# Kernel optimization log

Hardware: AMD Instinct MI355X
Metric: run time of the kernel (lower is better)

Reference implementation:

```python
import jax, jax.numpy as jnp
import numpy as np

B, D, FV, EMB, HID, E = 256, 1000, 300, 128, 128, 32000
NUM_LAYERS = 3


def _gcn_layer(h, src, tgt, W, b):
    # PyG GCNConv (add_self_loops=True, normalize=True) over N = h.shape[0] nodes.
    # NOTE: edges only reference nodes [0, D) (faithful to original forward),
    # but self-loops exist for all N nodes.
    N = h.shape[0]
    h = h @ W.T  # [N, out]
    deg = jnp.ones((N,), h.dtype).at[tgt].add(1.0)  # self-loop + in-degree
    dinv = deg ** -0.5
    coef = dinv[src] * dinv[tgt]  # [E]
    agg = jnp.zeros_like(h).at[tgt].add(h[src] * coef[:, None])
    agg = agg + h * (dinv * dinv)[:, None]  # self-loop messages
    return agg + b


def setup_inputs() -> dict:
    key = jax.random.key(0)
    ks = jax.random.split(key, 10)
    inp = {
        "X_num": jax.random.normal(ks[0], (B, 800), jnp.float32),
        "X_cat": jax.random.normal(ks[1], (B, 200), jnp.float32),
        "V": jax.random.normal(ks[2], (D, FV), jnp.float32),
        "edge_index": jax.random.randint(ks[3], (2, E), 0, D, jnp.int32),
        "W_embed": jax.random.normal(ks[4], (EMB, FV), jnp.float32) / np.sqrt(FV),
        "b_embed": jnp.zeros((EMB,), jnp.float32),
        "W0": jax.random.normal(ks[5], (HID, EMB), jnp.float32) / np.sqrt(EMB),
        "b0": jnp.zeros((HID,), jnp.float32),
        "W1": jax.random.normal(ks[6], (HID, HID), jnp.float32) / np.sqrt(HID),
        "b1": jnp.zeros((HID,), jnp.float32),
        "W2": jax.random.normal(ks[7], (HID, HID), jnp.float32) / np.sqrt(HID),
        "b2": jnp.zeros((HID,), jnp.float32),
    }
    return inp


def reference(X_num, X_cat, V, edge_index, W_embed, b_embed, W0, b0, W1, b1, W2, b2):
    x = jnp.concatenate([X_num, X_cat], axis=1)  # [B, D]
    emb = V @ W_embed.T + b_embed  # [D, EMB]
    h = x[:, :, None] * emb[None, :, :]  # [B, D, EMB]
    h = h.reshape(B * D, EMB)
    src, tgt = edge_index[0], edge_index[1]
    for W, b in ((W0, b0), (W1, b1), (W2, b2)):
        h = jax.nn.relu(_gcn_layer(h, src, tgt, W, b))
    h = h.reshape(B, D, HID)
    return h.mean(axis=1)  # conv_pool_method == 'mean'
```

## Files before the change

### kernel.cpp

```cpp
#include <hip/hip_runtime.h>
#include <hip/hip_bf16.h>

#define B_N 256
#define D_N 1000
#define H_N 128
#define E_N 32000
#define CAP 128

typedef unsigned int uint32;
typedef unsigned short u16;
typedef __attribute__((ext_vector_type(8))) short bf16x8;
typedef __attribute__((ext_vector_type(4))) float f32x4;

__device__ __forceinline__ u16 f2bf(float f) {
    union { float f; uint32 u; } v; v.f = f;
    return (u16)((v.u + 0x7fffu + ((v.u >> 16) & 1u)) >> 16);
}
__device__ __forceinline__ uint32 pk2(float lo, float hi) {
    __hip_bfloat162 h = __float22bfloat162_rn(make_float2(lo, hi));
    union { __hip_bfloat162 h; uint32 u; } v; v.h = h; return v.u;
}
__device__ __forceinline__ float asf(uint32 u) {
    union { uint32 u; float f; } v; v.u = u; return v.f;
}
__device__ __forceinline__ float rl(float x) { return x > 0.f ? x : 0.f; }

__device__ __forceinline__ void ld8g(const float* __restrict__ p, int kbase, float v[8]) {
    if (kbase + 8 <= 300) {
        float4 a = *(const float4*)p, b = *(const float4*)(p + 4);
        v[0] = a.x; v[1] = a.y; v[2] = a.z; v[3] = a.w;
        v[4] = b.x; v[5] = b.y; v[6] = b.z; v[7] = b.w;
    } else {
#pragma unroll
        for (int j = 0; j < 8; ++j) v[j] = (kbase + j < 300) ? p[j] : 0.f;
    }
}

__global__ void k_prep(const float* __restrict__ V, const float* __restrict__ W_embed,
                       const float* __restrict__ b_embed, const float* __restrict__ W0,
                       const float* __restrict__ Xn, const float* __restrict__ Xc,
                       const float* __restrict__ W1, const float* __restrict__ W2,
                       int* __restrict__ deg,
                       u16* __restrict__ w1h, u16* __restrict__ w2h,
                       u16* __restrict__ E1h, float* __restrict__ t0,
                       float* __restrict__ out) {
    __shared__ __align__(16) u16 sW0[128 * 128];
    __shared__ __align__(16) u16 sWc[128 * 64];
    __shared__ __align__(16) u16 sVc[16 * 64];
    __shared__ __align__(16) u16 sT[16 * 128];

    int bid = blockIdx.x, tid = threadIdx.x;
    if (bid >= 63) {
        if (bid < 127) {
            int i = (bid - 63) * 256 + tid;
            w1h[i] = f2bf(W1[i]); w2h[i] = f2bf(W2[i]);
        } else if (bid < 255) {
            int i = (bid - 127) * 256 + tid;
            out[i] = 0.f;
        } else {
            for (int j = tid; j < D_N; j += 256) deg[j] = 0;
        }
        return;
    }

    const int wave = tid >> 6, lane = tid & 63;
    const int quad = lane >> 4, l15 = lane & 15;
    const int nh = wave;
    const int dbase = bid * 16;

#pragma unroll
    for (int ii = 0; ii < 8; ++ii) {
        int idx = tid + ii * 256;
        int row = idx >> 4, g = idx & 15;
        float4 a = *(const float4*)(W0 + row * 128 + g * 8);
        float4 b = *(const float4*)(W0 + row * 128 + g * 8 + 4);
        uint4 pk = { pk2(a.x, a.y), pk2(a.z, a.w), pk2(b.x, b.y), pk2(b.z, b.w) };
        *(uint4*)&sW0[row * 128 + ((g ^ (row & 7)) << 3)] = pk;
    }

    f32x4 accA[2];
#pragma unroll
    for (int n = 0; n < 2; ++n) { accA[n][0] = 0.f; accA[n][1] = 0.f; accA[n][2] = 0.f; accA[n][3] = 0.f; }

    for (int ck = 0; ck < 5; ++ck) {
        int k0 = ck * 64;
        if (tid < 128) {
            int row = tid >> 3, seg = tid & 7;
            int d = dbase + row; int dc = d < D_N ? d : D_N - 1;
            int kk = k0 + seg * 8;
            float v[8]; ld8g(V + dc * 300 + kk, kk, v);
            uint4 pk = { pk2(v[0], v[1]), pk2(v[2], v[3]), pk2(v[4], v[5]), pk2(v[6], v[7]) };
            *(uint4*)&sVc[row * 64 + ((seg ^ (row & 7)) << 3)] = pk;
        }
#pragma unroll
        for (int gg = 0; gg < 4; ++gg) {
            int idx = tid + gg * 256;
            int row = idx >> 3, g = idx & 7;
            int kk = k0 + g * 8;
            float v[8]; ld8g(W_embed + row * 300 + kk, kk, v);
            uint4 pk = { pk2(v[0], v[1]), pk2(v[2], v[3]), pk2(v[4], v[5]), pk2(v[6], v[7]) };
            *(uint4*)&sWc[row * 64 + ((g ^ (row & 7)) << 3)] = pk;
        }
        __syncthreads();
#pragma unroll
        for (int ksb = 0; ksb < 2; ++ksb) {
            int g = ksb * 4 + quad;
            int ar = l15;
            bf16x8 av = *(const bf16x8*)&sVc[ar * 64 + ((g ^ (ar & 7)) << 3)];
#pragma unroll
            for (int n = 0; n < 2; ++n) {
                int br = nh * 32 + n * 16 + l15;
                bf16x8 bv = *(const bf16x8*)&sWc[br * 64 + ((g ^ (br & 7)) << 3)];
                accA[n] = __builtin_amdgcn_mfma_f32_16x16x32_bf16(av, bv, accA[n], 0, 0, 0);
            }
        }
        __syncthreads();
    }

    {
        const int odd = l15 & 1;
#pragma unroll
        for (int n = 0; n < 2; ++n) {
            float bb = b_embed[nh * 32 + n * 16 + l15];
            float v0 = accA[n][0] + bb, v1 = accA[n][1] + bb;
            float v2 = accA[n][2] + bb, v3 = accA[n][3] + bb;
            float t0_ = __shfl_xor(v0, 1), t1_ = __shfl_xor(v1, 1);
            float t2_ = __shfl_xor(v2, 1), t3_ = __shfl_xor(v3, 1);
            float lo0 = odd ? t2_ : v0, hi0 = odd ? v2 : t0_;
            float lo1 = odd ? t3_ : v1, hi1 = odd ? v3 : t1_;
            int r0 = quad * 4 + (odd ? 2 : 0);
            int r1 = r0 + 1;
            int ce = nh * 32 + n * 16 + (l15 & ~1);
            *(uint32*)&sT[r0 * 128 + (((ce >> 3) ^ (r0 & 7)) << 3) + (ce & 7)] = pk2(lo0, hi0);
            *(uint32*)&sT[r1 * 128 + (((ce >> 3) ^ (r1 & 7)) << 3) + (ce & 7)] = pk2(lo1, hi1);
        }
    }
    __syncthreads();

    f32x4 accB[2];
#pragma unroll
    for (int n = 0; n < 2; ++n) { accB[n][0] = 0.f; accB[n][1] = 0.f; accB[n][2] = 0.f; accB[n][3] = 0.f; }
#pragma unroll
    for (int ks = 0; ks < 4; ++ks) {
        int g = ks * 4 + quad;
        int ar = l15;
        bf16x8 av = *(const bf16x8*)&sT[ar * 128 + ((g ^ (ar & 7)) << 3)];
#pragma unroll
        for (int n = 0; n < 2; ++n) {
            int br = nh * 32 + n * 16 + l15;
            bf16x8 bv = *(const bf16x8*)&sW0[br * 128 + ((g ^ (br & 7)) << 3)];
            accB[n] = __builtin_amdgcn_mfma_f32_16x16x32_bf16(av, bv, accB[n], 0, 0, 0);
        }
    }

#pragma unroll
    for (int i = 0; i < 4; ++i) {
        int r = quad * 4 + i;
        int d = dbase + r;
        if (d < D_N) {
            float x0 = (d < 800) ? Xn[d] : Xc[d - 800];
#pragma unroll
            for (int n = 0; n < 2; ++n) {
                int col = nh * 32 + n * 16 + l15;
                float e1 = accB[n][i];
                E1h[d * H_N + col] = f2bf(e1);
                t0[d * H_N + col] = x0 * e1;
            }
        }
    }
}

__global__ void k_layer(const float* __restrict__ t_in, const float* __restrict__ bias,
                        const float* __restrict__ Wn, const int* __restrict__ deg,
                        const int* __restrict__ es,
                        float* __restrict__ t_out, float* out, int pool) {
    __shared__ float sh[128];
    int d = blockIdx.x, e = threadIdx.x;
    float di = rsqrtf(1.f + (float)deg[d]);
    float acc = t_in[d * H_N + e] * di * di;
    int n = deg[d]; if (n > CAP) n = CAP;
    const int* row = es + d * CAP;
    int i = 0;
    for (; i + 4 <= n; i += 4) {
        int a0 = row[i], a1 = row[i + 1], a2 = row[i + 2], a3 = row[i + 3];
        float c0 = rsqrtf(1.f + (float)deg[a0]);
        float c1 = rsqrtf(1.f + (float)deg[a1]);
        float c2 = rsqrtf(1.f + (float)deg[a2]);
        float c3 = rsqrtf(1.f + (float)deg[a3]);
        acc += di * (c0 * t_in[a0 * H_N + e] + c1 * t_in[a1 * H_N + e] +
                     c2 * t_in[a2 * H_N + e] + c3 * t_in[a3 * H_N + e]);
    }
    for (; i < n; ++i) {
        int s = row[i];
        acc += di * rsqrtf(1.f + (float)deg[s]) * t_in[s * H_N + e];
    }
    float h = rl(acc + bias[e]);
    if (pool) { atomicAdd(&out[e], h * (1.0f / 1000.0f)); return; }
    sh[e] = h;
    __syncthreads();
    const float4* hr = (const float4*)sh;
    const float4* wr = (const float4*)(Wn + e * 128);
    float s = 0.f;
#pragma unroll 8
    for (int k = 0; k < 32; ++k) {
        float4 a = hr[k], w = wr[k];
        s += a.x * w.x + a.y * w.y + a.z * w.z + a.w * w.w;
    }
    t_out[d * H_N + e] = s;
}

__global__ __launch_bounds__(256, 4)
void k_big(const float* __restrict__ Xn, const float* __restrict__ Xc,
           const u16* __restrict__ E1h, const u16* __restrict__ w1h,
           const u16* __restrict__ w2h, const float* __restrict__ b0,
           const float* __restrict__ b1, const float* __restrict__ b2,
           const int* __restrict__ eidx, int* __restrict__ deg,
           int* __restrict__ es, float* __restrict__ out) {
    __shared__ __align__(16) u16 sH[4 * 32 * 128];

    if (blockIdx.x < 125) {
        int e = blockIdx.x * 256 + threadIdx.x;
        int s = eidx[e], t = eidx[E_N + e];
        int pos = atomicAdd(&deg[t], 1);
        if (pos < CAP) es[t * CAP + pos] = s;
        return;
    }
    const int cb = blockIdx.x - 125;
    const int tid = threadIdx.x;
    const int wave = tid >> 6, lane = tid & 63;
    const int quad = lane >> 4, l15 = lane & 15;
    const int bi = 1 + (cb >> 3);
    const int mbase = ((cb & 7) << 7) + wave * 32;
    u16* hw = sH + wave * (32 * 128);

    const int rA = mbase + l15;  const int rAc = rA < D_N ? rA : D_N - 1;
    const int rB = rA + 16;      const int rBc = rB < D_N ? rB : D_N - 1;
    const float xvA = (rAc < 800) ? Xn[bi * 800 + rAc] : Xc[bi * 200 + rAc - 800];
    const float xvB = (rBc < 800) ? Xn[bi * 800 + rBc] : Xc[bi * 200 + rBc - 800];

    f32x4 acc[2][8];
#pragma unroll
    for (int rt = 0; rt < 2; ++rt)
#pragma unroll
        for (int n = 0; n < 8; ++n) {
            acc[rt][n][0] = 0.f; acc[rt][n][1] = 0.f;
            acc[rt][n][2] = 0.f; acc[rt][n][3] = 0.f;
        }

#pragma unroll
    for (int ks = 0; ks < 4; ++ks) {
        const int k8 = ks * 4 + quad;
        uint4 eA = *(const uint4*)(E1h + rAc * H_N + k8 * 8);
        uint4 eB = *(const uint4*)(E1h + rBc * H_N + k8 * 8);
        float4 bl = *(const float4*)(b0 + k8 * 8);
        float4 bh = *(const float4*)(b0 + k8 * 8 + 4);
        uint4 pA, pB;
        {
            float a0 = rl(fmaf(xvA, asf(eA.x << 16), bl.x));
            float a1 = rl(fmaf(xvA, asf(eA.x & 0xffff0000u), bl.y));
            float a2 = rl(fmaf(xvA, asf(eA.y << 16), bl.z));
            float a3 = rl(fmaf(xvA, asf(eA.y & 0xffff0000u), bl.w));
            float a4 = rl(fmaf(xvA, asf(eA.z << 16), bh.x));
            float a5 = rl(fmaf(xvA, asf(eA.z & 0xffff0000u), bh.y));
            float a6 = rl(fmaf(xvA, asf(eA.w << 16), bh.z));
            float a7 = rl(fmaf(xvA, asf(eA.w & 0xffff0000u), bh.w));
            pA = { pk2(a0, a1), pk2(a2, a3), pk2(a4, a5), pk2(a6, a7) };
            float c0 = rl(fmaf(xvB, asf(eB.x << 16), bl.x));
            float c1 = rl(fmaf(xvB, asf(eB.x & 0xffff0000u), bl.y));
            float c2 = rl(fmaf(xvB, asf(eB.y << 16), bl.z));
            float c3 = rl(fmaf(xvB, asf(eB.y & 0xffff0000u), bl.w));
            float c4 = rl(fmaf(xvB, asf(eB.z << 16), bh.x));
            float c5 = rl(fmaf(xvB, asf(eB.z & 0xffff0000u), bh.y));
            float c6 = rl(fmaf(xvB, asf(eB.w << 16), bh.z));
            float c7 = rl(fmaf(xvB, asf(eB.w & 0xffff0000u), bh.w));
            pB = { pk2(c0, c1), pk2(c2, c3), pk2(c4, c5), pk2(c6, c7) };
        }
        bf16x8 aA = *(const bf16x8*)&pA;
        bf16x8 aB = *(const bf16x8*)&pB;
#pragma unroll
        for (int n = 0; n < 8; ++n) {
            bf16x8 bw = *(const bf16x8*)(w1h + (n * 16 + l15) * H_N + k8 * 8);
            acc[0][n] = __builtin_amdgcn_mfma_f32_16x16x32_bf16(aA, bw, acc[0][n], 0, 0, 0);
            acc[1][n] = __builtin_amdgcn_mfma_f32_16x16x32_bf16(aB, bw, acc[1][n], 0, 0, 0);
        }
    }

    {
        const int odd = l15 & 1;
#pragma unroll
        for (int rt = 0; rt < 2; ++rt)
#pragma unroll
            for (int n = 0; n < 8; ++n) {
                float bg = b1[n * 16 + l15];
                float v0 = rl(acc[rt][n][0] + bg);
                float v1 = rl(acc[rt][n][1] + bg);
                float v2 = rl(acc[rt][n][2] + bg);
                float v3 = rl(acc[rt][n][3] + bg);
                float t0_ = __shfl_xor(v0, 1), t1_ = __shfl_xor(v1, 1);
                float t2_ = __shfl_xor(v2, 1), t3_ = __shfl_xor(v3, 1);
                float lo0 = odd ? t2_ : v0, hi0 = odd ? v2 : t0_;
                float lo1 = odd ? t3_ : v1, hi1 = odd ? v3 : t1_;
                int r0 = rt * 16 + quad * 4 + (odd ? 2 : 0);
                int r1 = r0 + 1;
                int ce = n * 16 + (l15 & ~1);
                *(uint32*)&hw[r0 * 128 + (((ce >> 3) ^ (r0 & 7)) << 3) + (ce & 7)] = pk2(lo0, hi0);
                *(uint32*)&hw[r1 * 128 + (((ce >> 3) ^ (r1 & 7)) << 3) + (ce & 7)] = pk2(lo1, hi1);
            }
    }

#pragma unroll
    for (int rt = 0; rt < 2; ++rt)
#pragma unroll
        for (int n = 0; n < 8; ++n) {
            acc[rt][n][0] = 0.f; acc[rt][n][1] = 0.f;
            acc[rt][n][2] = 0.f; acc[rt][n][3] = 0.f;
        }
#pragma unroll
    for (int ks = 0; ks < 4; ++ks) {
        int k8 = ks * 4 + quad;
        int m0 = l15, m1 = 16 + l15;
        bf16x8 a0 = *(const bf16x8*)&hw[m0 * 128 + ((k8 ^ (m0 & 7)) << 3)];
        bf16x8 a1 = *(const bf16x8*)&hw[m1 * 128 + ((k8 ^ (m1 & 7)) << 3)];
#pragma unroll
        for (int n = 0; n < 8; ++n) {
            bf16x8 bw = *(const bf16x8*)(w2h + (n * 16 + l15) * H_N + k8 * 8);
            acc[0][n] = __builtin_amdgcn_mfma_f32_16x16x32_bf16(a0, bw, acc[0][n], 0, 0, 0);
            acc[1][n] = __builtin_amdgcn_mfma_f32_16x16x32_bf16(a1, bw, acc[1][n], 0, 0, 0);
        }
    }

    int rem = D_N - mbase;
#pragma unroll
    for (int n = 0; n < 8; ++n) {
        float bg = b2[n * 16 + l15];
        float cs = 0.f;
#pragma unroll
        for (int rt = 0; rt < 2; ++rt)
#pragma unroll
            for (int i = 0; i < 4; ++i) {
                int r32 = rt * 16 + quad * 4 + i;
                float v = rl(acc[rt][n][i] + bg);
                if (r32 < rem) cs += v;
            }
        cs += __shfl_xor(cs, 16);
        cs += __shfl_xor(cs, 32);
        if (lane < 16) atomicAdd(&out[bi * H_N + n * 16 + l15], cs * (1.0f / 1000.0f));
    }
}

extern "C" void kernel_launch(void* const* d_in, const int* in_sizes, int n_in,
                              void* d_out, int out_size, void* d_ws, size_t ws_size,
                              hipStream_t stream) {
    const float* Xn = (const float*)d_in[0];
    const float* Xc = (const float*)d_in[1];
    const float* V = (const float*)d_in[2];
    const int* eidx = (const int*)d_in[3];
    const float* W_embed = (const float*)d_in[4];
    const float* b_embed = (const float*)d_in[5];
    const float* W0 = (const float*)d_in[6];
    const float* b0 = (const float*)d_in[7];
    const float* W1 = (const float*)d_in[8];
    const float* b1 = (const float*)d_in[9];
    const float* W2 = (const float*)d_in[10];
    const float* b2 = (const float*)d_in[11];
    float* out = (float*)d_out;

    char* p = (char*)d_ws;
    auto alloc = [&](size_t bytes) -> char* {
        char* r = p;
        p += (bytes + 255) & ~(size_t)255;
        return r;
    };
    u16*   E1h = (u16*)  alloc(D_N * H_N * 2);
    float* t0  = (float*)alloc(D_N * H_N * 4);
    float* t1  = (float*)alloc(D_N * H_N * 4);
    float* t2  = (float*)alloc(D_N * H_N * 4);
    u16*   w1h = (u16*)  alloc(H_N * H_N * 2);
    u16*   w2h = (u16*)  alloc(H_N * H_N * 2);
    int*   deg = (int*)  alloc(D_N * 4);
    int*   es  = (int*)  alloc(D_N * CAP * 4);

    k_prep<<<dim3(256), dim3(256), 0, stream>>>(V, W_embed, b_embed, W0, Xn, Xc,
                                                W1, W2, deg, w1h, w2h, E1h, t0, out);
    k_big<<<dim3(2165), dim3(256), 0, stream>>>(Xn, Xc, E1h, w1h, w2h, b0, b1, b2,
                                                eidx, deg, es, out);
    k_layer<<<dim3(1000), dim3(128), 0, stream>>>(t0, b0, W1, deg, es, t1, out, 0);
    k_layer<<<dim3(1000), dim3(128), 0, stream>>>(t1, b1, W2, deg, es, t2, out, 0);
    k_layer<<<dim3(1000), dim3(128), 0, stream>>>(t2, b2, (const float*)nullptr, deg, es,
                                                  (float*)nullptr, out, 1);
}
```

Measured before the change: 226.4 us.

## Fuse all stages into one persistent kernel with software grid barriers

Replaces the prep, big-MLP, and three GCN layer launches with a single persistent kernel of 512 blocks that synchronize through atomic grid barriers. W1 and W2 bf16 weights are staged in shared memory rather than read from global memory, and layer phases now process two nodes per 256-thread block. This removes inter-launch gaps and tail effects at the cost of spin-wait barriers and a co-residency requirement for all blocks.

```diff
diff --git a/kernel.cpp b/kernel.cpp
--- a/kernel.cpp
+++ b/kernel.cpp
@@ -6,6 +6,8 @@
 #define H_N 128
 #define E_N 32000
 #define CAP 128
+#define NBLK 512
+#define MAGIC 0x5eed5eed
 
 typedef unsigned int uint32;
 typedef unsigned short u16;
@@ -36,146 +38,25 @@
     }
 }
 
-__global__ void k_prep(const float* __restrict__ V, const float* __restrict__ W_embed,
-                       const float* __restrict__ b_embed, const float* __restrict__ W0,
-                       const float* __restrict__ Xn, const float* __restrict__ Xc,
-                       const float* __restrict__ W1, const float* __restrict__ W2,
-                       int* __restrict__ deg,
-                       u16* __restrict__ w1h, u16* __restrict__ w2h,
-                       u16* __restrict__ E1h, float* __restrict__ t0,
-                       float* __restrict__ out) {
-    __shared__ __align__(16) u16 sW0[128 * 128];
-    __shared__ __align__(16) u16 sWc[128 * 64];
-    __shared__ __align__(16) u16 sVc[16 * 64];
-    __shared__ __align__(16) u16 sT[16 * 128];
-
-    int bid = blockIdx.x, tid = threadIdx.x;
-    if (bid >= 63) {
-        if (bid < 127) {
-            int i = (bid - 63) * 256 + tid;
-            w1h[i] = f2bf(W1[i]); w2h[i] = f2bf(W2[i]);
-        } else if (bid < 255) {
-            int i = (bid - 127) * 256 + tid;
-            out[i] = 0.f;
-        } else {
-            for (int j = tid; j < D_N; j += 256) deg[j] = 0;
-        }
-        return;
-    }
-
-    const int wave = tid >> 6, lane = tid & 63;
-    const int quad = lane >> 4, l15 = lane & 15;
-    const int nh = wave;
-    const int dbase = bid * 16;
-
-#pragma unroll
-    for (int ii = 0; ii < 8; ++ii) {
-        int idx = tid + ii * 256;
-        int row = idx >> 4, g = idx & 15;
-        float4 a = *(const float4*)(W0 + row * 128 + g * 8);
-        float4 b = *(const float4*)(W0 + row * 128 + g * 8 + 4);
-        uint4 pk = { pk2(a.x, a.y), pk2(a.z, a.w), pk2(b.x, b.y), pk2(b.z, b.w) };
-        *(uint4*)&sW0[row * 128 + ((g ^ (row & 7)) << 3)] = pk;
-    }
-
-    f32x4 accA[2];
-#pragma unroll
-    for (int n = 0; n < 2; ++n) { accA[n][0] = 0.f; accA[n][1] = 0.f; accA[n][2] = 0.f; accA[n][3] = 0.f; }
-
-    for (int ck = 0; ck < 5; ++ck) {
-        int k0 = ck * 64;
-        if (tid < 128) {
-            int row = tid >> 3, seg = tid & 7;
-            int d = dbase + row; int dc = d < D_N ? d : D_N - 1;
-            int kk = k0 + seg * 8;
-            float v[8]; ld8g(V + dc * 300 + kk, kk, v);
-            uint4 pk = { pk2(v[0], v[1]), pk2(v[2], v[3]), pk2(v[4], v[5]), pk2(v[6], v[7]) };
-            *(uint4*)&sVc[row * 64 + ((seg ^ (row & 7)) << 3)] = pk;
-        }
-#pragma unroll
-        for (int gg = 0; gg < 4; ++gg) {
-            int idx = tid + gg * 256;
-            int row = idx >> 3, g = idx & 7;
-            int kk = k0 + g * 8;
-            float v[8]; ld8g(W_embed + row * 300 + kk, kk, v);
-            uint4 pk = { pk2(v[0], v[1]), pk2(v[2], v[3]), pk2(v[4], v[5]), pk2(v[6], v[7]) };
-            *(uint4*)&sWc[row * 64 + ((g ^ (row & 7)) << 3)] = pk;
-        }
-        __syncthreads();
-#pragma unroll
-        for (int ksb = 0; ksb < 2; ++ksb) {
-            int g = ksb * 4 + quad;
-            int ar = l15;
-            bf16x8 av = *(const bf16x8*)&sVc[ar * 64 + ((g ^ (ar & 7)) << 3)];
-#pragma unroll
-            for (int n = 0; n < 2; ++n) {
-                int br = nh * 32 + n * 16 + l15;
-                bf16x8 bv = *(const bf16x8*)&sWc[br * 64 + ((g ^ (br & 7)) << 3)];
-                accA[n] = __builtin_amdgcn_mfma_f32_16x16x32_bf16(av, bv, accA[n], 0, 0, 0);
-            }
-        }
-        __syncthreads();
-    }
-
-    {
-        const int odd = l15 & 1;
-#pragma unroll
-        for (int n = 0; n < 2; ++n) {
-            float bb = b_embed[nh * 32 + n * 16 + l15];
-            float v0 = accA[n][0] + bb, v1 = accA[n][1] + bb;
-            float v2 = accA[n][2] + bb, v3 = accA[n][3] + bb;
-            float t0_ = __shfl_xor(v0, 1), t1_ = __shfl_xor(v1, 1);
-            float t2_ = __shfl_xor(v2, 1), t3_ = __shfl_xor(v3, 1);
-            float lo0 = odd ? t2_ : v0, hi0 = odd ? v2 : t0_;
-            float lo1 = odd ? t3_ : v1, hi1 = odd ? v3 : t1_;
-            int r0 = quad * 4 + (odd ? 2 : 0);
-            int r1 = r0 + 1;
-            int ce = nh * 32 + n * 16 + (l15 & ~1);
-            *(uint32*)&sT[r0 * 128 + (((ce >> 3) ^ (r0 & 7)) << 3) + (ce & 7)] = pk2(lo0, hi0);
-            *(uint32*)&sT[r1 * 128 + (((ce >> 3) ^ (r1 & 7)) << 3) + (ce & 7)] = pk2(lo1, hi1);
-        }
-    }
+__device__ __forceinline__ void gbar(int* c) {
     __syncthreads();
-
-    f32x4 accB[2];
-#pragma unroll
-    for (int n = 0; n < 2; ++n) { accB[n][0] = 0.f; accB[n][1] = 0.f; accB[n][2] = 0.f; accB[n][3] = 0.f; }
-#pragma unroll
-    for (int ks = 0; ks < 4; ++ks) {
-        int g = ks * 4 + quad;
-        int ar = l15;
-        bf16x8 av = *(const bf16x8*)&sT[ar * 128 + ((g ^ (ar & 7)) << 3)];
-#pragma unroll
-        for (int n = 0; n < 2; ++n) {
-            int br = nh * 32 + n * 16 + l15;
-            bf16x8 bv = *(const bf16x8*)&sW0[br * 128 + ((g ^ (br & 7)) << 3)];
-            accB[n] = __builtin_amdgcn_mfma_f32_16x16x32_bf16(av, bv, accB[n], 0, 0, 0);
-        }
-    }
-
-#pragma unroll
-    for (int i = 0; i < 4; ++i) {
-        int r = quad * 4 + i;
-        int d = dbase + r;
-        if (d < D_N) {
-            float x0 = (d < 800) ? Xn[d] : Xc[d - 800];
-#pragma unroll
-            for (int n = 0; n < 2; ++n) {
-                int col = nh * 32 + n * 16 + l15;
-                float e1 = accB[n][i];
-                E1h[d * H_N + col] = f2bf(e1);
-                t0[d * H_N + col] = x0 * e1;
-            }
-        }
-    }
-}
-
-__global__ void k_layer(const float* __restrict__ t_in, const float* __restrict__ bias,
-                        const float* __restrict__ Wn, const int* __restrict__ deg,
-                        const int* __restrict__ es,
-                        float* __restrict__ t_out, float* out, int pool) {
-    __shared__ float sh[128];
-    int d = blockIdx.x, e = threadIdx.x;
+    if (threadIdx.x == 0) {
+        __threadfence();
+        __hip_atomic_fetch_add(c, 1, __ATOMIC_ACQ_REL, __HIP_MEMORY_SCOPE_AGENT);
+        while (__hip_atomic_load(c, __ATOMIC_ACQUIRE, __HIP_MEMORY_SCOPE_AGENT) < NBLK)
+            __builtin_amdgcn_s_sleep(8);
+    }
+    __syncthreads();
+}
+
+__device__ __forceinline__ void layer_b0(int u2, int tid,
+        const float* __restrict__ t_in, const float* __restrict__ bias,
+        const float* __restrict__ Wn, const int* __restrict__ deg,
+        const int* __restrict__ es, float* __restrict__ t_out,
+        float* out, int pool, float* shf) {
+    if (u2 >= 500) return;
+    int half = tid >> 7, e = tid & 127;
+    int d = u2 * 2 + half;
     float di = rsqrtf(1.f + (float)deg[d]);
     float acc = t_in[d * H_N + e] * di * di;
     int n = deg[d]; if (n > CAP) n = CAP;
@@ -196,9 +77,9 @@
     }
     float h = rl(acc + bias[e]);
     if (pool) { atomicAdd(&out[e], h * (1.0f / 1000.0f)); return; }
-    sh[e] = h;
+    shf[tid] = h;
     __syncthreads();
-    const float4* hr = (const float4*)sh;
+    const float4* hr = (const float4*)(shf + half * 128);
     const float4* wr = (const float4*)(Wn + e * 128);
     float s = 0.f;
 #pragma unroll 8
@@ -209,143 +90,310 @@
     t_out[d * H_N + e] = s;
 }
 
-__global__ __launch_bounds__(256, 4)
-void k_big(const float* __restrict__ Xn, const float* __restrict__ Xc,
-           const u16* __restrict__ E1h, const u16* __restrict__ w1h,
-           const u16* __restrict__ w2h, const float* __restrict__ b0,
-           const float* __restrict__ b1, const float* __restrict__ b2,
-           const int* __restrict__ eidx, int* __restrict__ deg,
-           int* __restrict__ es, float* __restrict__ out) {
-    __shared__ __align__(16) u16 sH[4 * 32 * 128];
-
-    if (blockIdx.x < 125) {
-        int e = blockIdx.x * 256 + threadIdx.x;
-        int s = eidx[e], t = eidx[E_N + e];
-        int pos = atomicAdd(&deg[t], 1);
-        if (pos < CAP) es[t * CAP + pos] = s;
-        return;
-    }
-    const int cb = blockIdx.x - 125;
-    const int tid = threadIdx.x;
+__global__ __launch_bounds__(256, 2)
+void k_mega(const float* __restrict__ Xn, const float* __restrict__ Xc,
+            const float* __restrict__ V, const int* __restrict__ eidx,
+            const float* __restrict__ W_embed, const float* __restrict__ b_embed,
+            const float* __restrict__ W0, const float* __restrict__ b0,
+            const float* __restrict__ W1, const float* __restrict__ b1,
+            const float* __restrict__ W2, const float* __restrict__ b2,
+            u16* __restrict__ w1h, u16* __restrict__ w2h,
+            u16* __restrict__ E1h, float* __restrict__ t0,
+            float* __restrict__ t1, float* __restrict__ t2,
+            int* __restrict__ deg, int* __restrict__ es,
+            int* bar, float* __restrict__ out) {
+    __shared__ __align__(16) unsigned char smem[65536];
+    u16* sA = (u16*)smem;
+    u16* sB = (u16*)(smem + 32768);
+
+    const int tid = threadIdx.x, bid = blockIdx.x;
     const int wave = tid >> 6, lane = tid & 63;
     const int quad = lane >> 4, l15 = lane & 15;
-    const int bi = 1 + (cb >> 3);
-    const int mbase = ((cb & 7) << 7) + wave * 32;
-    u16* hw = sH + wave * (32 * 128);
-
-    const int rA = mbase + l15;  const int rAc = rA < D_N ? rA : D_N - 1;
-    const int rB = rA + 16;      const int rBc = rB < D_N ? rB : D_N - 1;
-    const float xvA = (rAc < 800) ? Xn[bi * 800 + rAc] : Xc[bi * 200 + rAc - 800];
-    const float xvB = (rBc < 800) ? Xn[bi * 800 + rBc] : Xc[bi * 200 + rBc - 800];
-
-    f32x4 acc[2][8];
-#pragma unroll
-    for (int rt = 0; rt < 2; ++rt)
-#pragma unroll
-        for (int n = 0; n < 8; ++n) {
-            acc[rt][n][0] = 0.f; acc[rt][n][1] = 0.f;
-            acc[rt][n][2] = 0.f; acc[rt][n][3] = 0.f;
-        }
-
-#pragma unroll
-    for (int ks = 0; ks < 4; ++ks) {
-        const int k8 = ks * 4 + quad;
-        uint4 eA = *(const uint4*)(E1h + rAc * H_N + k8 * 8);
-        uint4 eB = *(const uint4*)(E1h + rBc * H_N + k8 * 8);
-        float4 bl = *(const float4*)(b0 + k8 * 8);
-        float4 bh = *(const float4*)(b0 + k8 * 8 + 4);
-        uint4 pA, pB;
+
+    if (bid == 0 && tid == 0) {
+        for (int i = 1; i <= 4; ++i)
+            __hip_atomic_store(bar + i, 0, __ATOMIC_RELAXED, __HIP_MEMORY_SCOPE_AGENT);
+        __hip_atomic_store(bar, MAGIC, __ATOMIC_RELEASE, __HIP_MEMORY_SCOPE_AGENT);
+    }
+
+    if (bid < 63) {
+        u16* sW0 = sA;
+        u16* sWc = sB;
+        u16* sVc = (u16*)(smem + 32768 + 16384);
+        u16* sT  = (u16*)(smem + 32768 + 16384 + 2048);
+        const int nh = wave;
+        const int dbase = bid * 16;
+#pragma unroll
+        for (int ii = 0; ii < 8; ++ii) {
+            int idx = tid + ii * 256;
+            int row = idx >> 4, g = idx & 15;
+            float4 a = *(const float4*)(W0 + row * 128 + g * 8);
+            float4 b = *(const float4*)(W0 + row * 128 + g * 8 + 4);
+            uint4 pk = { pk2(a.x, a.y), pk2(a.z, a.w), pk2(b.x, b.y), pk2(b.z, b.w) };
+            *(uint4*)&sW0[row * 128 + ((g ^ (row & 7)) << 3)] = pk;
+        }
+        f32x4 accA[2];
+#pragma unroll
+        for (int n = 0; n < 2; ++n) { accA[n][0]=0.f; accA[n][1]=0.f; accA[n][2]=0.f; accA[n][3]=0.f; }
+        for (int ck = 0; ck < 5; ++ck) {
+            int k0 = ck * 64;
+            if (tid < 128) {
+                int row = tid >> 3, seg = tid & 7;
+                int d = dbase + row; int dc = d < D_N ? d : D_N - 1;
+                int kk = k0 + seg * 8;
+                float v[8]; ld8g(V + dc * 300 + kk, kk, v);
+                uint4 pk = { pk2(v[0], v[1]), pk2(v[2], v[3]), pk2(v[4], v[5]), pk2(v[6], v[7]) };
+                *(uint4*)&sVc[row * 64 + ((seg ^ (row & 7)) << 3)] = pk;
+            }
+#pragma unroll
+            for (int gg = 0; gg < 4; ++gg) {
+                int idx = tid + gg * 256;
+                int row = idx >> 3, g = idx & 7;
+                int kk = k0 + g * 8;
+                float v[8]; ld8g(W_embed + row * 300 + kk, kk, v);
+                uint4 pk = { pk2(v[0], v[1]), pk2(v[2], v[3]), pk2(v[4], v[5]), pk2(v[6], v[7]) };
+                *(uint4*)&sWc[row * 64 + ((g ^ (row & 7)) << 3)] = pk;
+            }
+            __syncthreads();
+#pragma unroll
+            for (int ksb = 0; ksb < 2; ++ksb) {
+                int g = ksb * 4 + quad;
+                bf16x8 av = *(const bf16x8*)&sVc[l15 * 64 + ((g ^ (l15 & 7)) << 3)];
+#pragma unroll
+                for (int n = 0; n < 2; ++n) {
+                    int br = nh * 32 + n * 16 + l15;
+                    bf16x8 bv = *(const bf16x8*)&sWc[br * 64 + ((g ^ (br & 7)) << 3)];
+                    accA[n] = __builtin_amdgcn_mfma_f32_16x16x32_bf16(av, bv, accA[n], 0, 0, 0);
+                }
+            }
+            __syncthreads();
+        }
         {
-            float a0 = rl(fmaf(xvA, asf(eA.x << 16), bl.x));
-            float a1 = rl(fmaf(xvA, asf(eA.x & 0xffff0000u), bl.y));
-            float a2 = rl(fmaf(xvA, asf(eA.y << 16), bl.z));
-            float a3 = rl(fmaf(xvA, asf(eA.y & 0xffff0000u), bl.w));
-            float a4 = rl(fmaf(xvA, asf(eA.z << 16), bh.x));
-            float a5 = rl(fmaf(xvA, asf(eA.z & 0xffff0000u), bh.y));
-            float a6 = rl(fmaf(xvA, asf(eA.w << 16), bh.z));
-            float a7 = rl(fmaf(xvA, asf(eA.w & 0xffff0000u), bh.w));
-            pA = { pk2(a0, a1), pk2(a2, a3), pk2(a4, a5), pk2(a6, a7) };
-            float c0 = rl(fmaf(xvB, asf(eB.x << 16), bl.x));
-            float c1 = rl(fmaf(xvB, asf(eB.x & 0xffff0000u), bl.y));
-            float c2 = rl(fmaf(xvB, asf(eB.y << 16), bl.z));
-            float c3 = rl(fmaf(xvB, asf(eB.y & 0xffff0000u), bl.w));
-            float c4 = rl(fmaf(xvB, asf(eB.z << 16), bh.x));
-            float c5 = rl(fmaf(xvB, asf(eB.z & 0xffff0000u), bh.y));
-            float c6 = rl(fmaf(xvB, asf(eB.w << 16), bh.z));
-            float c7 = rl(fmaf(xvB, asf(eB.w & 0xffff0000u), bh.w));
-            pB = { pk2(c0, c1), pk2(c2, c3), pk2(c4, c5), pk2(c6, c7) };
-        }
-        bf16x8 aA = *(const bf16x8*)&pA;
-        bf16x8 aB = *(const bf16x8*)&pB;
-#pragma unroll
-        for (int n = 0; n < 8; ++n) {
-            bf16x8 bw = *(const bf16x8*)(w1h + (n * 16 + l15) * H_N + k8 * 8);
-            acc[0][n] = __builtin_amdgcn_mfma_f32_16x16x32_bf16(aA, bw, acc[0][n], 0, 0, 0);
-            acc[1][n] = __builtin_amdgcn_mfma_f32_16x16x32_bf16(aB, bw, acc[1][n], 0, 0, 0);
-        }
-    }
-
-    {
-        const int odd = l15 & 1;
-#pragma unroll
-        for (int rt = 0; rt < 2; ++rt)
-#pragma unroll
-            for (int n = 0; n < 8; ++n) {
-                float bg = b1[n * 16 + l15];
-                float v0 = rl(acc[rt][n][0] + bg);
-                float v1 = rl(acc[rt][n][1] + bg);
-                float v2 = rl(acc[rt][n][2] + bg);
-                float v3 = rl(acc[rt][n][3] + bg);
+            const int odd = l15 & 1;
+#pragma unroll
+            for (int n = 0; n < 2; ++n) {
+                float bb = b_embed[nh * 32 + n * 16 + l15];
+                float v0 = accA[n][0] + bb, v1 = accA[n][1] + bb;
+                float v2 = accA[n][2] + bb, v3 = accA[n][3] + bb;
                 float t0_ = __shfl_xor(v0, 1), t1_ = __shfl_xor(v1, 1);
                 float t2_ = __shfl_xor(v2, 1), t3_ = __shfl_xor(v3, 1);
                 float lo0 = odd ? t2_ : v0, hi0 = odd ? v2 : t0_;
                 float lo1 = odd ? t3_ : v1, hi1 = odd ? v3 : t1_;
-                int r0 = rt * 16 + quad * 4 + (odd ? 2 : 0);
+                int r0 = quad * 4 + (odd ? 2 : 0);
                 int r1 = r0 + 1;
-                int ce = n * 16 + (l15 & ~1);
-                *(uint32*)&hw[r0 * 128 + (((ce >> 3) ^ (r0 & 7)) << 3) + (ce & 7)] = pk2(lo0, hi0);
-                *(uint32*)&hw[r1 * 128 + (((ce >> 3) ^ (r1 & 7)) << 3) + (ce & 7)] = pk2(lo1, hi1);
-            }
-    }
-
-#pragma unroll
-    for (int rt = 0; rt < 2; ++rt)
-#pragma unroll
-        for (int n = 0; n < 8; ++n) {
-            acc[rt][n][0] = 0.f; acc[rt][n][1] = 0.f;
-            acc[rt][n][2] = 0.f; acc[rt][n][3] = 0.f;
-        }
-#pragma unroll
-    for (int ks = 0; ks < 4; ++ks) {
-        int k8 = ks * 4 + quad;
-        int m0 = l15, m1 = 16 + l15;
-        bf16x8 a0 = *(const bf16x8*)&hw[m0 * 128 + ((k8 ^ (m0 & 7)) << 3)];
-        bf16x8 a1 = *(const bf16x8*)&hw[m1 * 128 + ((k8 ^ (m1 & 7)) << 3)];
-#pragma unroll
-        for (int n = 0; n < 8; ++n) {
-            bf16x8 bw = *(const bf16x8*)(w2h + (n * 16 + l15) * H_N + k8 * 8);
-            acc[0][n] = __builtin_amdgcn_mfma_f32_16x16x32_bf16(a0, bw, acc[0][n], 0, 0, 0);
-            acc[1][n] = __builtin_amdgcn_mfma_f32_16x16x32_bf16(a1, bw, acc[1][n], 0, 0, 0);
-        }
-    }
-
-    int rem = D_N - mbase;
-#pragma unroll
-    for (int n = 0; n < 8; ++n) {
-        float bg = b2[n * 16 + l15];
-        float cs = 0.f;
-#pragma unroll
-        for (int rt = 0; rt < 2; ++rt)
-#pragma unroll
-            for (int i = 0; i < 4; ++i) {
-                int r32 = rt * 16 + quad * 4 + i;
-                float v = rl(acc[rt][n][i] + bg);
-                if (r32 < rem) cs += v;
-            }
-        cs += __shfl_xor(cs, 16);
-        cs += __shfl_xor(cs, 32);
-        if (lane < 16) atomicAdd(&out[bi * H_N + n * 16 + l15], cs * (1.0f / 1000.0f));
-    }
+                int ce = nh * 32 + n * 16 + (l15 & ~1);
+                *(uint32*)&sT[r0 * 128 + (((ce >> 3) ^ (r0 & 7)) << 3) + (ce & 7)] = pk2(lo0, hi0);
+                *(uint32*)&sT[r1 * 128 + (((ce >> 3) ^ (r1 & 7)) << 3) + (ce & 7)] = pk2(lo1, hi1);
+            }
+        }
+        __syncthreads();
+        f32x4 accB[2];
+#pragma unroll
+        for (int n = 0; n < 2; ++n) { accB[n][0]=0.f; accB[n][1]=0.f; accB[n][2]=0.f; accB[n][3]=0.f; }
+#pragma unroll
+        for (int ks = 0; ks < 4; ++ks) {
+            int g = ks * 4 + quad;
+            bf16x8 av = *(const bf16x8*)&sT[l15 * 128 + ((g ^ (l15 & 7)) << 3)];
+#pragma unroll
+            for (int n = 0; n < 2; ++n) {
+                int br = nh * 32 + n * 16 + l15;
+                bf16x8 bv = *(const bf16x8*)&sW0[br * 128 + ((g ^ (br & 7)) << 3)];
+                accB[n] = __builtin_amdgcn_mfma_f32_16x16x32_bf16(av, bv, accB[n], 0, 0, 0);
+            }
+        }
+#pragma unroll
+        for (int i = 0; i < 4; ++i) {
+            int r = quad * 4 + i;
+            int d = dbase + r;
+            if (d < D_N) {
+                float x0 = (d < 800) ? Xn[d] : Xc[d - 800];
+#pragma unroll
+                for (int n = 0; n < 2; ++n) {
+                    int col = nh * 32 + n * 16 + l15;
+                    float e1 = accB[n][i];
+                    E1h[d * H_N + col] = f2bf(e1);
+                    t0[d * H_N + col] = x0 * e1;
+                }
+            }
+        }
+    } else if (bid < 127) {
+        int i = (bid - 63) * 256 + tid;
+        w1h[i] = f2bf(W1[i]); w2h[i] = f2bf(W2[i]);
+    } else if (bid < 255) {
+        int i = (bid - 127) * 256 + tid;
+        out[i] = 0.f;
+    } else if (bid == 255) {
+        for (int j = tid; j < D_N; j += 256) deg[j] = 0;
+    }
+
+    __syncthreads();
+    if (tid == 0) {
+        while (__hip_atomic_load(bar, __ATOMIC_ACQUIRE, __HIP_MEMORY_SCOPE_AGENT) != MAGIC)
+            __builtin_amdgcn_s_sleep(8);
+        __threadfence();
+        __hip_atomic_fetch_add(bar + 1, 1, __ATOMIC_ACQ_REL, __HIP_MEMORY_SCOPE_AGENT);
+        while (__hip_atomic_load(bar + 1, __ATOMIC_ACQUIRE, __HIP_MEMORY_SCOPE_AGENT) < NBLK)
+            __builtin_amdgcn_s_sleep(8);
+    }
+    __syncthreads();
+
+    {
+        const uint4* w2v = (const uint4*)w2h;
+        for (int i = tid; i < 2048; i += 256) {
+            int row = i >> 4, g = i & 15;
+            *(uint4*)&sB[row * 128 + ((g ^ (row & 7)) << 3)] = w2v[i];
+        }
+        u16* hw = sA + wave * (32 * 128);
+
+        for (int u = bid; u < 2165; u += NBLK) {
+            if (u < 125) {
+                int e = u * 256 + tid;
+                int s = eidx[e], t = eidx[E_N + e];
+                int pos = atomicAdd(&deg[t], 1);
+                if (pos < CAP) es[t * CAP + pos] = s;
+                continue;
+            }
+            int c = u - 125;
+            int bi = 1 + (c >> 3);
+            int mbase = ((c & 7) << 7) + wave * 32;
+
+            __syncthreads();
+            const uint4* w1v = (const uint4*)w1h;
+#pragma unroll
+            for (int i = 0; i < 8; ++i) {
+                int idx = tid + i * 256;
+                int row = idx >> 4, g = idx & 15;
+                *(uint4*)&sA[row * 128 + ((g ^ (row & 7)) << 3)] = w1v[idx];
+            }
+            __syncthreads();
+
+            int rA = mbase + l15;  int rAc = rA < D_N ? rA : D_N - 1;
+            int rB = rA + 16;      int rBc = rB < D_N ? rB : D_N - 1;
+            float xvA = (rAc < 800) ? Xn[bi * 800 + rAc] : Xc[bi * 200 + rAc - 800];
+            float xvB = (rBc < 800) ? Xn[bi * 800 + rBc] : Xc[bi * 200 + rBc - 800];
+
+            f32x4 acc[2][8];
+#pragma unroll
+            for (int rt = 0; rt < 2; ++rt)
+#pragma unroll
+                for (int n = 0; n < 8; ++n) {
+                    acc[rt][n][0]=0.f; acc[rt][n][1]=0.f; acc[rt][n][2]=0.f; acc[rt][n][3]=0.f;
+                }
+
+#pragma unroll
+            for (int ks = 0; ks < 4; ++ks) {
+                const int k8 = ks * 4 + quad;
+                uint4 eA = *(const uint4*)(E1h + rAc * H_N + k8 * 8);
+                uint4 eB = *(const uint4*)(E1h + rBc * H_N + k8 * 8);
+                float4 bl = *(const float4*)(b0 + k8 * 8);
+                float4 bh = *(const float4*)(b0 + k8 * 8 + 4);
+                uint4 pA, pB;
+                {
+                    float a0 = rl(fmaf(xvA, asf(eA.x << 16), bl.x));
+                    float a1 = rl(fmaf(xvA, asf(eA.x & 0xffff0000u), bl.y));
+                    float a2 = rl(fmaf(xvA, asf(eA.y << 16), bl.z));
+                    float a3 = rl(fmaf(xvA, asf(eA.y & 0xffff0000u), bl.w));
+                    float a4 = rl(fmaf(xvA, asf(eA.z << 16), bh.x));
+                    float a5 = rl(fmaf(xvA, asf(eA.z & 0xffff0000u), bh.y));
+                    float a6 = rl(fmaf(xvA, asf(eA.w << 16), bh.z));
+                    float a7 = rl(fmaf(xvA, asf(eA.w & 0xffff0000u), bh.w));
+                    pA = { pk2(a0, a1), pk2(a2, a3), pk2(a4, a5), pk2(a6, a7) };
+                    float c0 = rl(fmaf(xvB, asf(eB.x << 16), bl.x));
+                    float c1 = rl(fmaf(xvB, asf(eB.x & 0xffff0000u), bl.y));
+                    float c2 = rl(fmaf(xvB, asf(eB.y << 16), bl.z));
+                    float c3 = rl(fmaf(xvB, asf(eB.y & 0xffff0000u), bl.w));
+                    float c4 = rl(fmaf(xvB, asf(eB.z << 16), bh.x));
+                    float c5 = rl(fmaf(xvB, asf(eB.z & 0xffff0000u), bh.y));
+                    float c6 = rl(fmaf(xvB, asf(eB.w << 16), bh.z));
+                    float c7 = rl(fmaf(xvB, asf(eB.w & 0xffff0000u), bh.w));
+                    pB = { pk2(c0, c1), pk2(c2, c3), pk2(c4, c5), pk2(c6, c7) };
+                }
+                bf16x8 aA = *(const bf16x8*)&pA;
+                bf16x8 aB = *(const bf16x8*)&pB;
+#pragma unroll
+                for (int n = 0; n < 8; ++n) {
+                    int br = n * 16 + l15;
+                    bf16x8 bw = *(const bf16x8*)&sA[br * 128 + ((k8 ^ (br & 7)) << 3)];
+                    acc[0][n] = __builtin_amdgcn_mfma_f32_16x16x32_bf16(aA, bw, acc[0][n], 0, 0, 0);
+                    acc[1][n] = __builtin_amdgcn_mfma_f32_16x16x32_bf16(aB, bw, acc[1][n], 0, 0, 0);
+                }
+            }
+
+            __syncthreads();
+
+            {
+                const int odd = l15 & 1;
+#pragma unroll
+                for (int rt = 0; rt < 2; ++rt)
+#pragma unroll
+                    for (int n = 0; n < 8; ++n) {
+                        float bg = b1[n * 16 + l15];
+                        float v0 = rl(acc[rt][n][0] + bg);
+                        float v1 = rl(acc[rt][n][1] + bg);
+                        float v2 = rl(acc[rt][n][2] + bg);
+                        float v3 = rl(acc[rt][n][3] + bg);
+                        float t0_ = __shfl_xor(v0, 1), t1_ = __shfl_xor(v1, 1);
+                        float t2_ = __shfl_xor(v2, 1), t3_ = __shfl_xor(v3, 1);
+                        float lo0 = odd ? t2_ : v0, hi0 = odd ? v2 : t0_;
+                        float lo1 = odd ? t3_ : v1, hi1 = odd ? v3 : t1_;
+                        int r0 = rt * 16 + quad * 4 + (odd ? 2 : 0);
+                        int r1 = r0 + 1;
+                        int ce = n * 16 + (l15 & ~1);
+                        *(uint32*)&hw[r0 * 128 + (((ce >> 3) ^ (r0 & 7)) << 3) + (ce & 7)] = pk2(lo0, hi0);
+                        *(uint32*)&hw[r1 * 128 + (((ce >> 3) ^ (r1 & 7)) << 3) + (ce & 7)] = pk2(lo1, hi1);
+                    }
+            }
+
+#pragma unroll
+            for (int rt = 0; rt < 2; ++rt)
+#pragma unroll
+                for (int n = 0; n < 8; ++n) {
+                    acc[rt][n][0]=0.f; acc[rt][n][1]=0.f; acc[rt][n][2]=0.f; acc[rt][n][3]=0.f;
+                }
+#pragma unroll
+            for (int ks = 0; ks < 4; ++ks) {
+                int k8 = ks * 4 + quad;
+                int m0 = l15, m1 = 16 + l15;
+                bf16x8 a0 = *(const bf16x8*)&hw[m0 * 128 + ((k8 ^ (m0 & 7)) << 3)];
+                bf16x8 a1 = *(const bf16x8*)&hw[m1 * 128 + ((k8 ^ (m1 & 7)) << 3)];
+#pragma unroll
+                for (int n = 0; n < 8; ++n) {
+                    int br = n * 16 + l15;
+                    bf16x8 bw = *(const bf16x8*)&sB[br * 128 + ((k8 ^ (br & 7)) << 3)];
+                    acc[0][n] = __builtin_amdgcn_mfma_f32_16x16x32_bf16(a0, bw, acc[0][n], 0, 0, 0);
+                    acc[1][n] = __builtin_amdgcn_mfma_f32_16x16x32_bf16(a1, bw, acc[1][n], 0, 0, 0);
+                }
+            }
+
+            int rem = D_N - mbase;
+#pragma unroll
+            for (int n = 0; n < 8; ++n) {
+                float bg = b2[n * 16 + l15];
+                float cs = 0.f;
+#pragma unroll
+                for (int rt = 0; rt < 2; ++rt)
+#pragma unroll
+                    for (int i = 0; i < 4; ++i) {
+                        int r32 = rt * 16 + quad * 4 + i;
+                        float v = rl(acc[rt][n][i] + bg);
+                        if (r32 < rem) cs += v;
+                    }
+                cs += __shfl_xor(cs, 16);
+                cs += __shfl_xor(cs, 32);
+                if (lane < 16) atomicAdd(&out[bi * H_N + n * 16 + l15], cs * (1.0f / 1000.0f));
+            }
+        }
+    }
+
+    gbar(bar + 2);
+
+    float* shf = (float*)smem;
+    layer_b0(bid, tid, t0, b0, W1, deg, es, t1, out, 0, shf);
+    gbar(bar + 3);
+    layer_b0(bid, tid, t1, b1, W2, deg, es, t2, out, 0, shf);
+    gbar(bar + 4);
+    layer_b0(bid, tid, t2, b2, (const float*)nullptr, deg, es,
+             (float*)nullptr, out, 1, shf);
 }
 
 extern "C" void kernel_launch(void* const* d_in, const int* in_sizes, int n_in,
@@ -379,13 +427,10 @@
     u16*   w2h = (u16*)  alloc(H_N * H_N * 2);
     int*   deg = (int*)  alloc(D_N * 4);
     int*   es  = (int*)  alloc(D_N * CAP * 4);
-
-    k_prep<<<dim3(256), dim3(256), 0, stream>>>(V, W_embed, b_embed, W0, Xn, Xc,
-                                                W1, W2, deg, w1h, w2h, E1h, t0, out);
-    k_big<<<dim3(2165), dim3(256), 0, stream>>>(Xn, Xc, E1h, w1h, w2h, b0, b1, b2,
-                                                eidx, deg, es, out);
-    k_layer<<<dim3(1000), dim3(128), 0, stream>>>(t0, b0, W1, deg, es, t1, out, 0);
-    k_layer<<<dim3(1000), dim3(128), 0, stream>>>(t1, b1, W2, deg, es, t2, out, 0);
-    k_layer<<<dim3(1000), dim3(128), 0, stream>>>(t2, b2, (const float*)nullptr, deg, es,
-                                                  (float*)nullptr, out, 1);
-}
+    int*   bar = (int*)  alloc(64);
+
+    k_mega<<<dim3(NBLK), dim3(256), 0, stream>>>(Xn, Xc, V, eidx, W_embed, b_embed,
+                                                 W0, b0, W1, b1, W2, b2,
+                                                 w1h, w2h, E1h, t0, t1, t2,
+                                                 deg, es, bar, out);
+}
```

New measurement: 460.4 us. 103% more time.
